# Kernel optimization log

Hardware: AMD Instinct MI355X
Metric: run time of the kernel (lower is better)

The kernel has to match this reference:

```python
import jax, jax.numpy as jnp
import numpy as np

B, C, T = 32, 1024, 1024
BETA = 0.95      # snn.Leaky(beta=0.95)
THR = 1.0        # snntorch Leaky default threshold
SIGMA_INIT = 10.5  # mean of sigma_range (1, 20)


def _gaussian_matrix(sigma, channels):
    # row i is the Gaussian pdf over x=0..C-1 centered at mean=i (vectorized
    # form of the source's per-row Python loop; identical values).
    x = jnp.arange(channels, dtype=jnp.float32)
    u = (x[None, :] - x[:, None]) / sigma  # [C, C]
    coef = 1.0 / (sigma * jnp.sqrt(jnp.asarray(2.0 * jnp.pi, dtype=jnp.float32)))
    return coef * jnp.exp(-0.5 * u * u)


def _spike(u):
    # heaviside(u) forward; ATan surrogate gradient (snntorch default, alpha=2)
    soft = jnp.arctan(jnp.pi * u) / jnp.pi
    hard = (u > 0).astype(u.dtype)
    return soft + jax.lax.stop_gradient(hard - soft)


def setup_inputs() -> dict:
    key = jax.random.key(0)
    inp = jax.random.normal(key, (B, C, T), dtype=jnp.float32)
    sigma = jnp.ones((1,), dtype=jnp.float32) * SIGMA_INIT
    return {"inp": inp, "sigma": sigma}


def reference(inp, sigma):
    # inp: [B, C, T], sigma: [1]
    s = sigma[0]
    w = _gaussian_matrix(s, inp.shape[1])  # computed once: identical at every t
    # I[b,i,t] = x[b,i,t] - sum_j w[i,j] * x[b,j,t]
    I = inp - jnp.einsum('ij,bjt->bit', w, inp)
    I_tbc = jnp.moveaxis(I, 2, 0)  # [T, B, C]

    def step(mem, It):
        # snntorch Leaky (reset_mechanism='subtract'):
        # reset fires on incoming mem, then decay+integrate, then spike.
        reset = _spike(mem - THR)
        mem = BETA * mem + It - reset * THR
        spk = _spike(mem - THR)
        return mem, spk

    mem0 = jnp.zeros(I_tbc.shape[1:], dtype=inp.dtype)  # [B, C]
    _, spks = jax.lax.scan(step, mem0, I_tbc)  # spks: [T, B, C]
    return jnp.moveaxis(spks, 0, 2)  # [B, C, T]
```

## Files before the change

kernel.cpp:

```cpp
#include <hip/hip_runtime.h>
#include <math.h>

#define B_     32
#define C_     1024
#define T_     1024
#define RT     92
#define CT     64
#define TT     64
#define KC     16
#define NTY    4
#define WOFF   (RT + KC - 1)
#define NWT    216
#define NCOLS  (CT + 2*RT)
#define XSTR   252
#define ISTR   65
#define NF4    (NCOLS * (TT/4))

__device__ __forceinline__ float tap_value(float s, int d) {
    float u    = __fdiv_rn((float)d, s);
    float t1   = __fmul_rn(-0.5f, u);
    float t2   = __fmul_rn(t1, u);
    float e    = (float)exp((double)t2);
    float den  = __fmul_rn(s, sqrtf(6.2831854820251465f));
    float coef = __fdiv_rn(1.0f, den);
    return __fmul_rn(coef, e);
}

#define EL(v, i) ((i) == 0 ? (v).x : (i) == 1 ? (v).y : (i) == 2 ? (v).z : (v).w)
#define SEL7(il, W0, W1, W2, W3, W4, W5, W6)                                    \
    ((il) < 4 ? EL(W0, (il)) : (il) < 8 ? EL(W1, (il) - 4)                      \
     : (il) < 12 ? EL(W2, (il) - 8) : (il) < 16 ? EL(W3, (il) - 12)             \
     : (il) < 20 ? EL(W4, (il) - 16) : (il) < 24 ? EL(W5, (il) - 20)            \
     : EL(W6, (il) - 24))

#define COL16(XV, CC, W0, W1, W2, W3, W4, W5, W6)                               \
    do {                                                                        \
        float x1_ = EL(XV, (CC) & 3);                                           \
        _Pragma("unroll")                                                       \
        for (int k = 0; k < KC; ++k) {                                          \
            const int il_ = (CC) + (KC - 1) - k;                                \
            acc[k] = fmaf(SEL7(il_, W0, W1, W2, W3, W4, W5, W6), x1_, acc[k]);  \
        }                                                                       \
    } while (0)

#define PASS(P)                                                                 \
    do {                                                                        \
        float4 w0 = TAPQ(3*(P)+0), w1 = TAPQ(3*(P)+1), w2 = TAPQ(3*(P)+2);      \
        float4 w3 = TAPQ(3*(P)+3), w4 = TAPQ(3*(P)+4), w5 = TAPQ(3*(P)+5);      \
        float4 w6 = TAPQ(3*(P)+6);                                              \
        float4 a0 = xq[3*(P)+0], a1 = xq[3*(P)+1], a2 = xq[3*(P)+2];            \
        COL16(a0, 0,  w0,w1,w2,w3,w4,w5,w6); COL16(a0, 1,  w0,w1,w2,w3,w4,w5,w6); \
        COL16(a0, 2,  w0,w1,w2,w3,w4,w5,w6); COL16(a0, 3,  w0,w1,w2,w3,w4,w5,w6); \
        COL16(a1, 4,  w0,w1,w2,w3,w4,w5,w6); COL16(a1, 5,  w0,w1,w2,w3,w4,w5,w6); \
        COL16(a1, 6,  w0,w1,w2,w3,w4,w5,w6); COL16(a1, 7,  w0,w1,w2,w3,w4,w5,w6); \
        COL16(a2, 8,  w0,w1,w2,w3,w4,w5,w6); COL16(a2, 9,  w0,w1,w2,w3,w4,w5,w6); \
        COL16(a2, 10, w0,w1,w2,w3,w4,w5,w6); COL16(a2, 11, w0,w1,w2,w3,w4,w5,w6); \
    } while (0)

#define PASSL()                                                                 \
    do {                                                                        \
        float4 w0 = TAPQ(48), w1 = TAPQ(49), w2 = TAPQ(50);                     \
        float4 w3 = TAPQ(51), w4 = TAPQ(52), w5 = TAPQ(53);                     \
        float4 a0 = xq[48], a1 = xq[49];                                        \
        COL16(a0, 0, w0,w1,w2,w3,w4,w5,w5); COL16(a0, 1, w0,w1,w2,w3,w4,w5,w5); \
        COL16(a0, 2, w0,w1,w2,w3,w4,w5,w5); COL16(a0, 3, w0,w1,w2,w3,w4,w5,w5); \
        COL16(a1, 4, w0,w1,w2,w3,w4,w5,w5); COL16(a1, 5, w0,w1,w2,w3,w4,w5,w5); \
        COL16(a1, 6, w0,w1,w2,w3,w4,w5,w5); COL16(a1, 7, w0,w1,w2,w3,w4,w5,w5); \
    } while (0)

__global__ __launch_bounds__(256)
__attribute__((amdgpu_waves_per_eu(2, 4))) void snn_v15(
    const float* __restrict__ x, const float* __restrict__ sigma,
    float* __restrict__ out)
{
    __shared__ __align__(16) float xsT[TT * XSTR];
    __shared__ __align__(16) float IsS[NTY * KC * ISTR];

    const int tx   = threadIdx.x;
    const int ty   = threadIdx.y;
    const int flat = ty * 64 + tx;
    const int b    = blockIdx.y;
    const int c0   = blockIdx.x * CT;
    const int rb   = ty * KC;

    const float* xb = x   + (size_t)b * ((size_t)C_ * T_);
    float*       ob = out + (size_t)b * ((size_t)C_ * T_);

    if (flat < NWT) {
        int d = flat - WOFF;
        xsT[(flat >> 2) * XSTR + 248 + (flat & 3)] =
            (d >= -RT && d <= RT) ? tap_value(sigma[0], d) : 0.0f;
    }

    float4 stg[16];

#define STAGE_LOAD(T0)                                                          \
    _Pragma("unroll")                                                           \
    for (int i = 0; i < 16; ++i) {                                              \
        int e = flat + i * 256;                                                 \
        float4 v = make_float4(0.f, 0.f, 0.f, 0.f);                             \
        if (e < NF4) {                                                          \
            int r = e >> 4, c4 = e & 15;                                        \
            int c = c0 - RT + r;                                                \
            if (c >= 0 && c < C_)                                               \
                v = *(const float4*)(xb + (size_t)c * T_ + (T0) + c4 * 4);      \
        }                                                                       \
        stg[i] = v;                                                             \
    }

#define STAGE_WRITE()                                                           \
    _Pragma("unroll")                                                           \
    for (int i = 0; i < 16; ++i) {                                              \
        int e = flat + i * 256;                                                 \
        if (e < NF4) {                                                          \
            int r = e >> 4, c4 = e & 15;                                        \
            xsT[(4 * c4 + 0) * XSTR + r] = stg[i].x;                            \
            xsT[(4 * c4 + 1) * XSTR + r] = stg[i].y;                            \
            xsT[(4 * c4 + 2) * XSTR + r] = stg[i].z;                            \
            xsT[(4 * c4 + 3) * XSTR + r] = stg[i].w;                            \
        }                                                                       \
    }

#define TAPQ(Q) (*(const float4*)(xsT + (Q) * XSTR + 248))

    STAGE_LOAD(0);

    float mem = 0.0f;
    float rc  = 0.0f;
    float* strip = IsS + ty * (KC * ISTR);
    const float4* xq = (const float4*)(xsT + tx * XSTR + rb);

#pragma unroll 1
    for (int kk = 0; kk < T_ / TT; ++kk) {
        STAGE_WRITE();
        __syncthreads();

        if (kk < T_ / TT - 1) { STAGE_LOAD((kk + 1) * TT); }

        float acc[KC];
#pragma unroll
        for (int k = 0; k < KC; ++k) acc[k] = 0.0f;

        PASS(0);  PASS(1);  PASS(2);  PASS(3);
        PASS(4);  PASS(5);  PASS(6);  PASS(7);
        PASS(8);  PASS(9);  PASS(10); PASS(11);
        PASS(12); PASS(13); PASS(14); PASS(15);
        PASSL();

        {
            float4 xo0 = xq[23], xo1 = xq[24], xo2 = xq[25], xo3 = xq[26];
            strip[ 0 * ISTR + tx] = __fsub_rn(xo0.x, acc[0]);
            strip[ 1 * ISTR + tx] = __fsub_rn(xo0.y, acc[1]);
            strip[ 2 * ISTR + tx] = __fsub_rn(xo0.z, acc[2]);
            strip[ 3 * ISTR + tx] = __fsub_rn(xo0.w, acc[3]);
            strip[ 4 * ISTR + tx] = __fsub_rn(xo1.x, acc[4]);
            strip[ 5 * ISTR + tx] = __fsub_rn(xo1.y, acc[5]);
            strip[ 6 * ISTR + tx] = __fsub_rn(xo1.z, acc[6]);
            strip[ 7 * ISTR + tx] = __fsub_rn(xo1.w, acc[7]);
            strip[ 8 * ISTR + tx] = __fsub_rn(xo2.x, acc[8]);
            strip[ 9 * ISTR + tx] = __fsub_rn(xo2.y, acc[9]);
            strip[10 * ISTR + tx] = __fsub_rn(xo2.z, acc[10]);
            strip[11 * ISTR + tx] = __fsub_rn(xo2.w, acc[11]);
            strip[12 * ISTR + tx] = __fsub_rn(xo3.x, acc[12]);
            strip[13 * ISTR + tx] = __fsub_rn(xo3.y, acc[13]);
            strip[14 * ISTR + tx] = __fsub_rn(xo3.z, acc[14]);
            strip[15 * ISTR + tx] = __fsub_rn(xo3.w, acc[15]);
        }

        if (tx < KC) {
            float m = mem, r = rc;
            const float* srow = strip + tx * ISTR;
            float* orow = ob + (size_t)(c0 + rb + tx) * T_ + (size_t)kk * TT;
#pragma unroll 4
            for (int q = 0; q < TT / 4; ++q) {
                float4 s;
#pragma unroll
                for (int qq = 0; qq < 4; ++qq) {
                    float Ivv = srow[4 * q + qq];
                    m = __fsub_rn(__fadd_rn(__fmul_rn(0.95f, m), Ivv), r);
                    float sp = (m > 1.0f) ? 1.0f : 0.0f;
                    r = sp;
                    if (qq == 0) s.x = sp; else if (qq == 1) s.y = sp;
                    else if (qq == 2) s.z = sp; else s.w = sp;
                }
                *(float4*)(orow + 4 * q) = s;
            }
            mem = m; rc = r;
        }
        __syncthreads();
    }
#undef STAGE_LOAD
#undef STAGE_WRITE
#undef TAPQ
}

extern "C" void kernel_launch(void* const* d_in, const int* in_sizes, int n_in,
                              void* d_out, int out_size, void* d_ws, size_t ws_size,
                              hipStream_t stream) {
    const float* x     = (const float*)d_in[0];
    const float* sigma = (const float*)d_in[1];
    float* out = (float*)d_out;

    dim3 grid(C_ / CT, B_);
    dim3 block(64, NTY);

    snn_v15<<<grid, block, 0, stream>>>(x, sigma, out);
}
```

Baseline: 206.7 us.

## Warp-specialize block into ping-pong groups overlapping conv, scan, and loads

The block is split into two groups of two waves that alternate roles each 32-step time chunk. One group computes the Gaussian convolution into its strip. The other group runs the serial leaky-integrate scan on the previous chunk with one wave and loads the next chunk into its own buffer with the other. The goal is to hide the serial recurrence and global loads behind the convolution math instead of serializing them per tile. The cost is half the threads doing the FMA work per phase, smaller time tiles, more barriers, and dropping the waves_per_eu hint.

```diff
diff --git a/kernel.cpp b/kernel.cpp
--- a/kernel.cpp
+++ b/kernel.cpp
@@ -6,15 +6,14 @@
 #define T_     1024
 #define RT     92
 #define CT     64
-#define TT     64
+#define TTC    32
 #define KC     16
-#define NTY    4
 #define WOFF   (RT + KC - 1)
 #define NWT    216
 #define NCOLS  (CT + 2*RT)
 #define XSTR   252
-#define ISTR   65
-#define NF4    (NCOLS * (TT/4))
+#define ISTR   33
+#define NQ4    (NCOLS * (TTC/4))
 
 __device__ __forceinline__ float tap_value(float s, int d) {
     float u    = __fdiv_rn((float)d, s);
@@ -42,6 +41,9 @@
             acc[k] = fmaf(SEL7(il_, W0, W1, W2, W3, W4, W5, W6), x1_, acc[k]);  \
         }                                                                       \
     } while (0)
+
+#define TAPQ(Q)                                                                 \
+    (*(const float4*)(((Q) < 32 ? xsA + (Q) * XSTR : xsB + ((Q) - 32) * XSTR) + 248))
 
 #define PASS(P)                                                                 \
     do {                                                                        \
@@ -68,130 +70,136 @@
         COL16(a1, 6, w0,w1,w2,w3,w4,w5,w5); COL16(a1, 7, w0,w1,w2,w3,w4,w5,w5); \
     } while (0)
 
-__global__ __launch_bounds__(256)
-__attribute__((amdgpu_waves_per_eu(2, 4))) void snn_v15(
+__global__ __launch_bounds__(256) void snn_v20(
     const float* __restrict__ x, const float* __restrict__ sigma,
     float* __restrict__ out)
 {
-    __shared__ __align__(16) float xsT[TT * XSTR];
-    __shared__ __align__(16) float IsS[NTY * KC * ISTR];
+    __shared__ __align__(16) float xsA[TTC * XSTR];
+    __shared__ __align__(16) float xsB[TTC * XSTR];
+    __shared__ __align__(16) float stripA[CT * ISTR];
+    __shared__ __align__(16) float stripB[CT * ISTR];
+    __shared__ float mem_lds[CT];
 
     const int tx   = threadIdx.x;
     const int ty   = threadIdx.y;
     const int flat = ty * 64 + tx;
+    const int g    = ty >> 1;
+    const int wg   = ty & 1;
     const int b    = blockIdx.y;
     const int c0   = blockIdx.x * CT;
-    const int rb   = ty * KC;
 
     const float* xb = x   + (size_t)b * ((size_t)C_ * T_);
     float*       ob = out + (size_t)b * ((size_t)C_ * T_);
 
     if (flat < NWT) {
         int d = flat - WOFF;
-        xsT[(flat >> 2) * XSTR + 248 + (flat & 3)] =
-            (d >= -RT && d <= RT) ? tap_value(sigma[0], d) : 0.0f;
+        float w = (d >= -RT && d <= RT) ? tap_value(sigma[0], d) : 0.0f;
+        int q = flat >> 2, e = flat & 3;
+        float* dst = (q < 32) ? (xsA + q * XSTR + 248 + e)
+                              : (xsB + (q - 32) * XSTR + 248 + e);
+        *dst = w;
     }
-
-    float4 stg[16];
-
-#define STAGE_LOAD(T0)                                                          \
-    _Pragma("unroll")                                                           \
-    for (int i = 0; i < 16; ++i) {                                              \
-        int e = flat + i * 256;                                                 \
-        float4 v = make_float4(0.f, 0.f, 0.f, 0.f);                             \
-        if (e < NF4) {                                                          \
-            int r = e >> 4, c4 = e & 15;                                        \
-            int c = c0 - RT + r;                                                \
-            if (c >= 0 && c < C_)                                               \
-                v = *(const float4*)(xb + (size_t)c * T_ + (T0) + c4 * 4);      \
-        }                                                                       \
-        stg[i] = v;                                                             \
+    if (flat < CT) mem_lds[flat] = 0.0f;
+#pragma unroll
+    for (int i = 0; i < 8; ++i) {
+        int e = flat + i * 256;
+        if (e < NQ4) {
+            int r = e >> 3, c4 = e & 7;
+            int c = c0 - RT + r;
+            float4 v = make_float4(0.f, 0.f, 0.f, 0.f);
+            if (c >= 0 && c < C_)
+                v = *(const float4*)(xb + (size_t)c * T_ + c4 * 4);
+            xsA[(4 * c4 + 0) * XSTR + r] = v.x;
+            xsA[(4 * c4 + 1) * XSTR + r] = v.y;
+            xsA[(4 * c4 + 2) * XSTR + r] = v.z;
+            xsA[(4 * c4 + 3) * XSTR + r] = v.w;
+        }
     }
-
-#define STAGE_WRITE()                                                           \
-    _Pragma("unroll")                                                           \
-    for (int i = 0; i < 16; ++i) {                                              \
-        int e = flat + i * 256;                                                 \
-        if (e < NF4) {                                                          \
-            int r = e >> 4, c4 = e & 15;                                        \
-            xsT[(4 * c4 + 0) * XSTR + r] = stg[i].x;                            \
-            xsT[(4 * c4 + 1) * XSTR + r] = stg[i].y;                            \
-            xsT[(4 * c4 + 2) * XSTR + r] = stg[i].z;                            \
-            xsT[(4 * c4 + 3) * XSTR + r] = stg[i].w;                            \
-        }                                                                       \
-    }
-
-#define TAPQ(Q) (*(const float4*)(xsT + (Q) * XSTR + 248))
-
-    STAGE_LOAD(0);
-
-    float mem = 0.0f;
-    float rc  = 0.0f;
-    float* strip = IsS + ty * (KC * ISTR);
-    const float4* xq = (const float4*)(xsT + tx * XSTR + rb);
+    __syncthreads();
+
+    const int tloc = tx & 31;
+    const int rb   = ((tx >> 5) + 2 * wg) * 16;
+    float* bufg    = (g == 0) ? xsA : xsB;
+    float* stripg  = (g == 0) ? stripA : stripB;
+    const float4* xq = (const float4*)(bufg + tloc * XSTR + rb);
 
 #pragma unroll 1
-    for (int kk = 0; kk < T_ / TT; ++kk) {
-        STAGE_WRITE();
-        __syncthreads();
-
-        if (kk < T_ / TT - 1) { STAGE_LOAD((kk + 1) * TT); }
-
-        float acc[KC];
-#pragma unroll
-        for (int k = 0; k < KC; ++k) acc[k] = 0.0f;
-
-        PASS(0);  PASS(1);  PASS(2);  PASS(3);
-        PASS(4);  PASS(5);  PASS(6);  PASS(7);
-        PASS(8);  PASS(9);  PASS(10); PASS(11);
-        PASS(12); PASS(13); PASS(14); PASS(15);
-        PASSL();
-
-        {
-            float4 xo0 = xq[23], xo1 = xq[24], xo2 = xq[25], xo3 = xq[26];
-            strip[ 0 * ISTR + tx] = __fsub_rn(xo0.x, acc[0]);
-            strip[ 1 * ISTR + tx] = __fsub_rn(xo0.y, acc[1]);
-            strip[ 2 * ISTR + tx] = __fsub_rn(xo0.z, acc[2]);
-            strip[ 3 * ISTR + tx] = __fsub_rn(xo0.w, acc[3]);
-            strip[ 4 * ISTR + tx] = __fsub_rn(xo1.x, acc[4]);
-            strip[ 5 * ISTR + tx] = __fsub_rn(xo1.y, acc[5]);
-            strip[ 6 * ISTR + tx] = __fsub_rn(xo1.z, acc[6]);
-            strip[ 7 * ISTR + tx] = __fsub_rn(xo1.w, acc[7]);
-            strip[ 8 * ISTR + tx] = __fsub_rn(xo2.x, acc[8]);
-            strip[ 9 * ISTR + tx] = __fsub_rn(xo2.y, acc[9]);
-            strip[10 * ISTR + tx] = __fsub_rn(xo2.z, acc[10]);
-            strip[11 * ISTR + tx] = __fsub_rn(xo2.w, acc[11]);
-            strip[12 * ISTR + tx] = __fsub_rn(xo3.x, acc[12]);
-            strip[13 * ISTR + tx] = __fsub_rn(xo3.y, acc[13]);
-            strip[14 * ISTR + tx] = __fsub_rn(xo3.z, acc[14]);
-            strip[15 * ISTR + tx] = __fsub_rn(xo3.w, acc[15]);
-        }
-
-        if (tx < KC) {
-            float m = mem, r = rc;
-            const float* srow = strip + tx * ISTR;
-            float* orow = ob + (size_t)(c0 + rb + tx) * T_ + (size_t)kk * TT;
-#pragma unroll 4
-            for (int q = 0; q < TT / 4; ++q) {
-                float4 s;
-#pragma unroll
-                for (int qq = 0; qq < 4; ++qq) {
-                    float Ivv = srow[4 * q + qq];
-                    m = __fsub_rn(__fadd_rn(__fmul_rn(0.95f, m), Ivv), r);
-                    float sp = (m > 1.0f) ? 1.0f : 0.0f;
-                    r = sp;
-                    if (qq == 0) s.x = sp; else if (qq == 1) s.y = sp;
-                    else if (qq == 2) s.z = sp; else s.w = sp;
+    for (int m = 0; m <= 32; ++m) {
+        if (m <= 31 && g == (m & 1)) {
+            float acc[KC];
+#pragma unroll
+            for (int k = 0; k < KC; ++k) acc[k] = 0.0f;
+
+            PASS(0);  PASS(1);  PASS(2);  PASS(3);
+            PASS(4);  PASS(5);  PASS(6);  PASS(7);
+            PASS(8);  PASS(9);  PASS(10); PASS(11);
+            PASS(12); PASS(13); PASS(14); PASS(15);
+            PASSL();
+
+            {
+                float4 xo0 = xq[23], xo1 = xq[24], xo2 = xq[25], xo3 = xq[26];
+                stripg[(rb +  0) * ISTR + tloc] = __fsub_rn(xo0.x, acc[0]);
+                stripg[(rb +  1) * ISTR + tloc] = __fsub_rn(xo0.y, acc[1]);
+                stripg[(rb +  2) * ISTR + tloc] = __fsub_rn(xo0.z, acc[2]);
+                stripg[(rb +  3) * ISTR + tloc] = __fsub_rn(xo0.w, acc[3]);
+                stripg[(rb +  4) * ISTR + tloc] = __fsub_rn(xo1.x, acc[4]);
+                stripg[(rb +  5) * ISTR + tloc] = __fsub_rn(xo1.y, acc[5]);
+                stripg[(rb +  6) * ISTR + tloc] = __fsub_rn(xo1.z, acc[6]);
+                stripg[(rb +  7) * ISTR + tloc] = __fsub_rn(xo1.w, acc[7]);
+                stripg[(rb +  8) * ISTR + tloc] = __fsub_rn(xo2.x, acc[8]);
+                stripg[(rb +  9) * ISTR + tloc] = __fsub_rn(xo2.y, acc[9]);
+                stripg[(rb + 10) * ISTR + tloc] = __fsub_rn(xo2.z, acc[10]);
+                stripg[(rb + 11) * ISTR + tloc] = __fsub_rn(xo2.w, acc[11]);
+                stripg[(rb + 12) * ISTR + tloc] = __fsub_rn(xo3.x, acc[12]);
+                stripg[(rb + 13) * ISTR + tloc] = __fsub_rn(xo3.y, acc[13]);
+                stripg[(rb + 14) * ISTR + tloc] = __fsub_rn(xo3.z, acc[14]);
+                stripg[(rb + 15) * ISTR + tloc] = __fsub_rn(xo3.w, acc[15]);
+            }
+        } else if (m <= 32 && g != (m & 1)) {
+            if (wg == 0) {
+                if (m >= 1) {
+                    float mv = mem_lds[tx];
+                    float r  = (mv > 1.0f) ? 1.0f : 0.0f;
+                    const float* srow = stripg + tx * ISTR;
+                    float* orow = ob + (size_t)(c0 + tx) * T_ + (size_t)(m - 1) * TTC;
+#pragma unroll
+                    for (int q = 0; q < TTC / 4; ++q) {
+                        float4 s;
+#pragma unroll
+                        for (int qq = 0; qq < 4; ++qq) {
+                            float Ivv = srow[4 * q + qq];
+                            mv = __fsub_rn(__fadd_rn(__fmul_rn(0.95f, mv), Ivv), r);
+                            float sp = (mv > 1.0f) ? 1.0f : 0.0f;
+                            r = sp;
+                            if (qq == 0) s.x = sp; else if (qq == 1) s.y = sp;
+                            else if (qq == 2) s.z = sp; else s.w = sp;
+                        }
+                        *(float4*)(orow + 4 * q) = s;
+                    }
+                    mem_lds[tx] = mv;
                 }
-                *(float4*)(orow + 4 * q) = s;
+            } else {
+                if (m + 1 <= 31) {
+                    const int t0s = (m + 1) * TTC;
+                    const int r0  = tx >> 3, c40 = tx & 7;
+                    const int cb  = c0 - RT + r0;
+#pragma unroll
+                    for (int i = 0; i < 31; ++i) {
+                        int c = cb + 8 * i;
+                        float4 v = make_float4(0.f, 0.f, 0.f, 0.f);
+                        if (c >= 0 && c < C_)
+                            v = *(const float4*)(xb + (size_t)c * T_ + t0s + c40 * 4);
+                        int ra = r0 + 8 * i;
+                        bufg[(4 * c40 + 0) * XSTR + ra] = v.x;
+                        bufg[(4 * c40 + 1) * XSTR + ra] = v.y;
+                        bufg[(4 * c40 + 2) * XSTR + ra] = v.z;
+                        bufg[(4 * c40 + 3) * XSTR + ra] = v.w;
+                    }
+                }
             }
-            mem = m; rc = r;
         }
         __syncthreads();
     }
-#undef STAGE_LOAD
-#undef STAGE_WRITE
-#undef TAPQ
 }
 
 extern "C" void kernel_launch(void* const* d_in, const int* in_sizes, int n_in,
@@ -202,7 +210,7 @@
     float* out = (float*)d_out;
 
     dim3 grid(C_ / CT, B_);
-    dim3 block(64, NTY);
-
-    snn_v15<<<grid, block, 0, stream>>>(x, sigma, out);
+    dim3 block(64, 4);
+
+    snn_v20<<<grid, block, 0, stream>>>(x, sigma, out);
 }
```

New measurement: 340.3 us. 64.6% more time.
